# Kernel tuning notes

Measured on AMD Instinct MI355X. Metric: run time of the kernel, lower is better.

The kernel has to match this reference:

```python
import jax, jax.numpy as jnp
import numpy as np

# Static config (matches init_kwargs)
B, S = 4, 1024            # prefill: 4 sequences of 1024 tokens (num_tokens = 4096)
H = 16                    # num_heads
NOPE, ROPE, VD = 128, 64, 128
RANK = 512                # kv_lora_rank
SCALE = 0.07216878364870323  # 1/sqrt(head_dim=192)


def setup_inputs() -> dict:
    key = jax.random.key(0)
    k1, k2, k3, k4 = jax.random.split(key, 4)
    T = B * S
    return {
        "q": jax.random.normal(k1, (T, H, NOPE + ROPE), dtype=jnp.float32),
        "compressed_kv": jax.random.normal(k2, (T, RANK), dtype=jnp.float32),
        "rope_k": jax.random.normal(k3, (T, ROPE), dtype=jnp.float32),
        "w_up": jax.random.normal(k4, (H * (NOPE + VD), RANK), dtype=jnp.float32) * 0.02,
    }


def reference(q, compressed_kv, rope_k, w_up):
    T = q.shape[0]
    # Up-project latent -> per-head (k_nope, v): [T, H, NOPE+VD]
    kv = (compressed_kv @ w_up.T).reshape(B, S, H, NOPE + VD)
    k_nope = kv[..., :NOPE]          # [B,S,H,NOPE]
    v = kv[..., NOPE:]               # [B,S,H,VD]

    qb = q.reshape(B, S, H, NOPE + ROPE)
    q_nope = qb[..., :NOPE]          # [B,S,H,NOPE]
    q_rope = qb[..., NOPE:]          # [B,S,H,ROPE]
    rk = rope_k.reshape(B, S, ROPE)  # head-shared RoPE K component

    # Attention logits: nope part (per-head K) + rope part (shared K)
    scores = jnp.einsum('bqhd,bkhd->bhqk', q_nope, k_nope)
    scores = scores + jnp.einsum('bqhd,bkd->bhqk', q_rope, rk)
    scores = scores * SCALE

    # Causal mask within each sequence
    causal = jnp.tril(jnp.ones((S, S), dtype=bool))
    scores = jnp.where(causal[None, None], scores, jnp.finfo(scores.dtype).min)

    p = jax.nn.softmax(scores, axis=-1)                 # [B,H,S,S]
    out = jnp.einsum('bhqk,bkhd->bqhd', p, v)           # [B,S,H,VD]
    return out.reshape(T, H, VD)
```

## Files before the change

kernel.cpp:

```cpp
#include <hip/hip_runtime.h>
#include <stdint.h>


#define Hz 16
#define Sz 1024
#define RANKz 512
#define SCALEf 0.07216878364870323f

typedef unsigned short u16;
typedef __attribute__((ext_vector_type(8))) short bf16x8;
typedef __attribute__((ext_vector_type(4))) float f32x4;
typedef __attribute__((ext_vector_type(16))) float f32x16;

__device__ __forceinline__ u16 f2b(float f) {
  union { float f; uint32_t u; } x; x.f = f;
  return (u16)((x.u + 0x7fffu + ((x.u >> 16) & 1u)) >> 16);
}
__device__ __forceinline__ uint32_t cvtpk(float lo, float hi_) {
  uint32_t r;
  asm("v_cvt_pk_bf16_f32 %0, %1, %2" : "=v"(r) : "v"(lo), "v"(hi_));
  return r;
}

__global__ void cvt_bf16_kernel(const float* __restrict__ a, u16* __restrict__ ao,
                                const float* __restrict__ b, u16* __restrict__ bo,
                                const float* __restrict__ c, u16* __restrict__ co,
                                int na, int nb) {
  int idx = blockIdx.x * blockDim.x + threadIdx.x;
  const float* s; u16* d; int i;
  if (idx < na)            { s = a; d = ao; i = idx; }
  else if (idx < na + nb)  { s = b; d = bo; i = idx - na; }
  else                     { s = c; d = co; i = idx - na - nb; }
  float4 v = ((const float4*)s)[i];
  ushort4 o = make_ushort4(f2b(v.x), f2b(v.y), f2b(v.z), f2b(v.w));
  ((ushort4*)d)[i] = o;
}

__global__ __launch_bounds__(256)
void gemm_kv_bf16(const u16* __restrict__ A,
                  const u16* __restrict__ Bm,
                  u16* __restrict__ C) {
  __shared__ u16 As[128 * 32];
  __shared__ u16 Bs[128 * 32];
  const int tid = threadIdx.x;
  const int w = tid >> 6, lane = tid & 63;
  const int wr = w >> 1, wc = w & 1;
  const int row0 = blockIdx.x * 128, col0 = blockIdx.y * 128;
  f32x4 acc[4][4];
#pragma unroll
  for (int m = 0; m < 4; ++m)
#pragma unroll
    for (int n = 0; n < 4; ++n) acc[m][n] = (f32x4){0.f, 0.f, 0.f, 0.f};

  const int rstage = (lane >> 2);
  const int cstage = (lane & 3) * 8;

  for (int kt = 0; kt < RANKz / 32; ++kt) {
    const int k0 = kt * 32;
#pragma unroll
    for (int i = 0; i < 2; ++i) {
      const int chunk = i * 4 + w;
      const int r = chunk * 16 + rstage;
      const u16* ga = A  + (size_t)(row0 + r) * RANKz + k0 + cstage;
      const u16* gb = Bm + (size_t)(col0 + r) * RANKz + k0 + cstage;
      __builtin_amdgcn_global_load_lds((const __attribute__((address_space(1))) void*)ga,
                                       (__attribute__((address_space(3))) void*)&As[chunk * 512], 16, 0, 0);
      __builtin_amdgcn_global_load_lds((const __attribute__((address_space(1))) void*)gb,
                                       (__attribute__((address_space(3))) void*)&Bs[chunk * 512], 16, 0, 0);
    }
    __syncthreads();
    const int klo = (lane >> 4) * 8;
    bf16x8 af[4], bfr[4];
#pragma unroll
    for (int m = 0; m < 4; ++m)
      af[m] = *(const bf16x8*)&As[(wr * 64 + m * 16 + (lane & 15)) * 32 + klo];
#pragma unroll
    for (int n = 0; n < 4; ++n)
      bfr[n] = *(const bf16x8*)&Bs[(wc * 64 + n * 16 + (lane & 15)) * 32 + klo];
#pragma unroll
    for (int m = 0; m < 4; ++m)
#pragma unroll
      for (int n = 0; n < 4; ++n)
        acc[m][n] = __builtin_amdgcn_mfma_f32_16x16x32_bf16(af[m], bfr[n], acc[m][n], 0, 0, 0);
    __syncthreads();
  }
  const int cb = col0 + wc * 64 + (lane & 15);
  const int rb = row0 + wr * 64 + (lane >> 4) * 4;
#pragma unroll
  for (int m = 0; m < 4; ++m)
#pragma unroll
    for (int n = 0; n < 4; ++n)
#pragma unroll
      for (int j = 0; j < 4; ++j)
        C[(size_t)(rb + m * 16 + j) * 4096 + (cb + n * 16)] = f2b(acc[m][n][j]);
}

__global__ __launch_bounds__(512, 2)
void mla_attn_mfma(const float* __restrict__ q,
                   const u16* __restrict__ kvb,
                   const u16* __restrict__ ropeb,
                   float* __restrict__ out) {
  __shared__ __align__(16) unsigned char LB[131072];

  const int tid = threadIdx.x;
  const int w = tid >> 6, lane = tid & 63;
  const int l31 = lane & 31, hi = lane >> 5;
  const int half = w >> 2, strip = w & 3;

  const int bid = blockIdx.x;
  const int job = (bid & 7) * 32 + (bid >> 3);
  const int bh = job >> 2, pr = job & 3;
  const int bat = bh >> 4, h = bh & 15;
  const int tok0 = bat * Sz;

  const int vkp = tid & 63, vdc = (tid >> 6) & 7;

#pragma unroll 1
  for (int pass = 0; pass < 2; ++pass) {
    const int qt = pass ? pr : (7 - pr);
    const int ntiles = qt + 1;
    const int q0 = qt * 128 + strip * 32;

    bf16x8 qf[12];
    {
      const float* qp = q + ((size_t)(tok0 + q0 + l31) * Hz + h) * 192 + hi * 8;
#pragma unroll
      for (int ds = 0; ds < 12; ++ds) {
        float4 a = *(const float4*)(qp + ds * 16);
        float4 b = *(const float4*)(qp + ds * 16 + 4);
        union { bf16x8 v; u16 u[8]; } t;
        t.u[0] = f2b(a.x * SCALEf); t.u[1] = f2b(a.y * SCALEf);
        t.u[2] = f2b(a.z * SCALEf); t.u[3] = f2b(a.w * SCALEf);
        t.u[4] = f2b(b.x * SCALEf); t.u[5] = f2b(b.y * SCALEf);
        t.u[6] = f2b(b.z * SCALEf); t.u[7] = f2b(b.w * SCALEf);
        qf[ds] = t.v;
      }
    }

    f32x16 acc[4];
#pragma unroll
    for (int db = 0; db < 4; ++db)
#pragma unroll
      for (int r = 0; r < 16; ++r) acc[db][r] = 0.f;
    float m_run = -1e30f, l_run = 0.f;

    uint4 va0, va1, vb0, vb1;

    {
      const int tokt = tok0;
#pragma unroll
      for (int i = 0; i < 4; ++i) {
        const int c = w * 4 + i;
        const int row = c * 4 + (lane >> 4);
        const int sc = (lane & 15) ^ (row & 7);
        const u16* src = kvb + ((size_t)(tokt + row) * Hz + h) * 256 + sc * 8;
        __builtin_amdgcn_global_load_lds((const __attribute__((address_space(1))) void*)src,
                                         (__attribute__((address_space(3))) void*)(LB + c * 1024), 16, 0, 0);
      }
#pragma unroll
      for (int i = 0; i < 2; ++i) {
        const int c = w * 2 + i;
        const int row = c * 8 + (lane >> 3);
        const int sc = (lane & 7) ^ (row & 7);
        const u16* src = ropeb + (size_t)(tokt + row) * 64 + sc * 8;
        __builtin_amdgcn_global_load_lds((const __attribute__((address_space(1))) void*)src,
                                         (__attribute__((address_space(3))) void*)(LB + 65536 + c * 1024), 16, 0, 0);
      }
      const u16* vp = kvb + ((size_t)(tokt + vkp * 2) * Hz + h) * 256 + 128 + vdc * 16;
      va0 = *(const uint4*)(vp);
      va1 = *(const uint4*)(vp + 8);
      vb0 = *(const uint4*)(vp + Hz * 256);
      vb1 = *(const uint4*)(vp + Hz * 256 + 8);
    }
    __syncthreads();
    {
      union { uint4 v; u16 u[8]; } A0, A1, B0, B1;
      A0.v = va0; A1.v = va1; B0.v = vb0; B1.v = vb1;
      char* vt = (char*)(LB + 98304);
      const int inb = (4 * vkp) & 15, cc = vkp >> 2;
#pragma unroll
      for (int i = 0; i < 8; ++i) {
        { const int d = vdc * 16 + i;
          uint32_t wv = (uint32_t)A0.u[i] | ((uint32_t)B0.u[i] << 16);
          *(uint32_t*)(vt + d * 256 + 16 * (cc ^ (d & 7)) + inb) = wv; }
        { const int d = vdc * 16 + 8 + i;
          uint32_t wv = (uint32_t)A1.u[i] | ((uint32_t)B1.u[i] << 16);
          *(uint32_t*)(vt + d * 256 + 16 * (cc ^ (d & 7)) + inb) = wv; }
      }
    }
    __syncthreads();

#pragma unroll 1
    for (int t = 0; t < ntiles; ++t) {
      const int cur = t & 1;
      const bool havenext = (t + 1 < ntiles);
      if (havenext) {
        const int tokt = tok0 + (t + 1) * 128;
#pragma unroll
        for (int i = 0; i < 4; ++i) {
          const int c = w * 4 + i;
          const int row = c * 4 + (lane >> 4);
          const int sc = (lane & 15) ^ (row & 7);
          const u16* src = kvb + ((size_t)(tokt + row) * Hz + h) * 256 + sc * 8;
          __builtin_amdgcn_global_load_lds((const __attribute__((address_space(1))) void*)src,
                                           (__attribute__((address_space(3))) void*)(LB + (cur ^ 1) * 32768 + c * 1024), 16, 0, 0);
        }
#pragma unroll
        for (int i = 0; i < 2; ++i) {
          const int c = w * 2 + i;
          const int row = c * 8 + (lane >> 3);
          const int sc = (lane & 7) ^ (row & 7);
          const u16* src = ropeb + (size_t)(tokt + row) * 64 + sc * 8;
          __builtin_amdgcn_global_load_lds((const __attribute__((address_space(1))) void*)src,
                                           (__attribute__((address_space(3))) void*)(LB + 65536 + (cur ^ 1) * 16384 + c * 1024), 16, 0, 0);
        }
        const u16* vp = kvb + ((size_t)(tokt + vkp * 2) * Hz + h) * 256 + 128 + vdc * 16;
        va0 = *(const uint4*)(vp);
        va1 = *(const uint4*)(vp + 8);
        vb0 = *(const uint4*)(vp + Hz * 256);
        vb1 = *(const uint4*)(vp + Hz * 256 + 8);
      }

      const bool active = (t * 128 + half * 64) <= (q0 + 31);
      if (active) {
        const u16* KnC = (const u16*)(LB + cur * 32768);
        const u16* KrC = (const u16*)(LB + 65536 + cur * 16384);
        f32x16 s0, s1;
#pragma unroll
        for (int r = 0; r < 16; ++r) { s0[r] = 0.f; s1[r] = 0.f; }
        const int row_a = half * 64 + l31;
        const int row_b = row_a + 32;
#pragma unroll
        for (int ds = 0; ds < 8; ++ds) {
          bf16x8 k0v = *(const bf16x8*)&KnC[row_a * 128 + 8 * ((2 * ds + hi) ^ (row_a & 7))];
          bf16x8 k1v = *(const bf16x8*)&KnC[row_b * 128 + 8 * ((2 * ds + hi) ^ (row_b & 7))];
          s0 = __builtin_amdgcn_mfma_f32_32x32x16_bf16(k0v, qf[ds], s0, 0, 0, 0);
          s1 = __builtin_amdgcn_mfma_f32_32x32x16_bf16(k1v, qf[ds], s1, 0, 0, 0);
        }
#pragma unroll
        for (int ds = 8; ds < 12; ++ds) {
          bf16x8 k0v = *(const bf16x8*)&KrC[row_a * 64 + 8 * ((2 * (ds - 8) + hi) ^ (row_a & 7))];
          bf16x8 k1v = *(const bf16x8*)&KrC[row_b * 64 + 8 * ((2 * (ds - 8) + hi) ^ (row_b & 7))];
          s0 = __builtin_amdgcn_mfma_f32_32x32x16_bf16(k0v, qf[ds], s0, 0, 0, 0);
          s1 = __builtin_amdgcn_mfma_f32_32x32x16_bf16(k1v, qf[ds], s1, 0, 0, 0);
        }

        if (t == qt) {
          const int qg = q0 + l31;
          const int kb0 = t * 128 + half * 64;
#pragma unroll
          for (int r = 0; r < 16; ++r) {
            const int cr_ = (r & 3) + 8 * (r >> 2) + 4 * hi;
            if (kb0 + cr_ > qg)      s0[r] = -1e30f;
            if (kb0 + 32 + cr_ > qg) s1[r] = -1e30f;
          }
        }

        float mx = -1e30f;
#pragma unroll
        for (int r = 0; r < 16; ++r) { mx = fmaxf(mx, s0[r]); mx = fmaxf(mx, s1[r]); }
        mx = fmaxf(mx, __shfl_xor(mx, 32));
        const bool need = __any(mx > m_run + 8.f);
        if (need) {
          const float nm = fmaxf(m_run, mx);
          const float cr = __expf(m_run - nm);
          m_run = nm; l_run *= cr;
#pragma unroll
          for (int r = 0; r < 16; ++r) {
            const float crg = __shfl(cr, (r & 3) + 8 * (r >> 2) + 4 * hi);
#pragma unroll
            for (int db = 0; db < 4; ++db) acc[db][r] *= crg;
          }
        }
        float ts = 0.f;
#pragma unroll
        for (int r = 0; r < 16; ++r) {
          s0[r] = __expf(s0[r] - m_run); ts += s0[r];
          s1[r] = __expf(s1[r] - m_run); ts += s1[r];
        }
        ts += __shfl_xor(ts, 32);
        l_run += ts;

        bf16x8 pf[4];
#pragma unroll
        for (int ks = 0; ks < 4; ++ks) {
          const int o = (ks & 1) * 8;
          uint32_t w0, w1, w2, w3;
          if (ks < 2) {
            w0 = cvtpk(s0[o + 0], s0[o + 1]); w1 = cvtpk(s0[o + 4], s0[o + 5]);
            w2 = cvtpk(s0[o + 2], s0[o + 3]); w3 = cvtpk(s0[o + 6], s0[o + 7]);
          } else {
            w0 = cvtpk(s1[o + 0], s1[o + 1]); w1 = cvtpk(s1[o + 4], s1[o + 5]);
            w2 = cvtpk(s1[o + 2], s1[o + 3]); w3 = cvtpk(s1[o + 6], s1[o + 7]);
          }
          const uint32_t t0 = __shfl_xor(w0, 32), t1 = __shfl_xor(w1, 32);
          const uint32_t t2 = __shfl_xor(w2, 32), t3 = __shfl_xor(w3, 32);
          union { bf16x8 v; uint32_t u[4]; } P;
          P.u[0] = hi ? t1 : w0;
          P.u[1] = hi ? t3 : w2;
          P.u[2] = hi ? w1 : t0;
          P.u[3] = hi ? w3 : t2;
          pf[ks] = P.v;
        }

        const u16* VtC = (const u16*)(LB + 98304);
#pragma unroll
        for (int ks = 0; ks < 4; ++ks)
#pragma unroll
          for (int db = 0; db < 4; ++db) {
            const int row = db * 32 + l31;
            bf16x8 vf = *(const bf16x8*)&VtC[row * 128 + 8 * ((half * 8 + 2 * ks + hi) ^ (row & 7))];
            acc[db] = __builtin_amdgcn_mfma_f32_32x32x16_bf16(pf[ks], vf, acc[db], 0, 0, 0);
          }
      }

      __syncthreads();
      if (havenext) {
        union { uint4 v; u16 u[8]; } A0, A1, B0, B1;
        A0.v = va0; A1.v = va1; B0.v = vb0; B1.v = vb1;
        char* vt = (char*)(LB + 98304);
        const int inb = (4 * vkp) & 15, cc = vkp >> 2;
#pragma unroll
        for (int i = 0; i < 8; ++i) {
          { const int d = vdc * 16 + i;
            uint32_t wv = (uint32_t)A0.u[i] | ((uint32_t)B0.u[i] << 16);
            *(uint32_t*)(vt + d * 256 + 16 * (cc ^ (d & 7)) + inb) = wv; }
          { const int d = vdc * 16 + 8 + i;
            uint32_t wv = (uint32_t)A1.u[i] | ((uint32_t)B1.u[i] << 16);
            *(uint32_t*)(vt + d * 256 + 16 * (cc ^ (d & 7)) + inb) = wv; }
        }
        __syncthreads();
      }
    }

    float* mb = (float*)LB;
    float* ml = (float*)(LB + 65536);
    if (half == 1) {
#pragma unroll
      for (int db = 0; db < 4; ++db)
#pragma unroll
        for (int q4 = 0; q4 < 4; ++q4) {
          float4 v = make_float4(acc[db][q4 * 4 + 0], acc[db][q4 * 4 + 1],
                                 acc[db][q4 * 4 + 2], acc[db][q4 * 4 + 3]);
          *(float4*)&mb[strip * 4096 + db * 1024 + q4 * 256 + lane * 4] = v;
        }
      if (lane < 32) { ml[strip * 64 + lane] = m_run; ml[strip * 64 + 32 + lane] = l_run; }
    }
    __syncthreads();
    if (half == 0) {
      const float mp = ml[strip * 64 + l31];
      const float lp = ml[strip * 64 + 32 + l31];
      const float M  = fmaxf(m_run, mp);
      const float sA = __expf(m_run - M);
      const float sB = __expf(mp - M);
      const float inv = 1.0f / (l_run * sA + lp * sB);
      const float fAl = sA * inv, fBl = sB * inv;
      float fA[16], fB[16];
#pragma unroll
      for (int r = 0; r < 16; ++r) {
        const int cr_ = (r & 3) + 8 * (r >> 2) + 4 * hi;
        fA[r] = __shfl(fAl, cr_);
        fB[r] = __shfl(fBl, cr_);
      }
#pragma unroll
      for (int db = 0; db < 4; ++db)
#pragma unroll
        for (int q4 = 0; q4 < 4; ++q4) {
          float4 pv = *(const float4*)&mb[strip * 4096 + db * 1024 + q4 * 256 + lane * 4];
#pragma unroll
          for (int jj = 0; jj < 4; ++jj) {
            const int r = q4 * 4 + jj;
            const int cr_ = (r & 3) + 8 * (r >> 2) + 4 * hi;
            const float pvj = (jj == 0) ? pv.x : (jj == 1) ? pv.y : (jj == 2) ? pv.z : pv.w;
            out[((size_t)(tok0 + q0 + cr_) * Hz + h) * 128 + db * 32 + l31] =
                acc[db][r] * fA[r] + pvj * fB[r];
          }
        }
    }
    __syncthreads();
  }
}

extern "C" void kernel_launch(void* const* d_in, const int* in_sizes, int n_in,
                              void* d_out, int out_size, void* d_ws, size_t ws_size,
                              hipStream_t stream) {
  const float* q    = (const float*)d_in[0];
  const float* ckv  = (const float*)d_in[1];
  const float* rope = (const float*)d_in[2];
  const float* wup  = (const float*)d_in[3];
  float* out = (float*)d_out;

  u16* ckvb  = (u16*)d_ws;
  u16* wupb  = ckvb + (size_t)4096 * RANKz;
  u16* kvb   = wupb + (size_t)4096 * RANKz;
  u16* ropeb = kvb + (size_t)4096 * 4096;

  const int nvec = 4096 * RANKz / 4;
  const int nrope = 4096 * 64 / 4;
  cvt_bf16_kernel<<<(2 * nvec + nrope) / 256, 256, 0, stream>>>(ckv, ckvb, wup, wupb, rope, ropeb, nvec, nvec);

  dim3 gg(32, 32);
  gemm_kv_bf16<<<gg, 256, 0, stream>>>(ckvb, wupb, kvb);

  mla_attn_mfma<<<256, 512, 0, stream>>>(q, kvb, ropeb, out);
}
```

Before: 90.00 us.

## Split attention key tile across four wave quarters with 1024-thread blocks

Doubles the attention block to 16 waves so each wave handles 32 keys of a 128-key tile instead of 64. The four partial softmax/PV results per query strip are then merged through LDS in a two-step tree, with partials stored as bf16. Wave priority is raised around the MFMA sections. The aim is more waves in flight to hide latency, at the cost of extra merge work, lower-precision partials, and tighter register limits that could cause spills.

```diff
diff --git a/kernel.cpp b/kernel.cpp
--- a/kernel.cpp
+++ b/kernel.cpp
@@ -6,6 +6,7 @@
 #define Sz 1024
 #define RANKz 512
 #define SCALEf 0.07216878364870323f
+#define CRr(r) ((((r) & 3)) + 8 * ((r) >> 2) + 4 * hi)
 
 typedef unsigned short u16;
 typedef __attribute__((ext_vector_type(8))) short bf16x8;
@@ -15,6 +16,10 @@
 __device__ __forceinline__ u16 f2b(float f) {
   union { float f; uint32_t u; } x; x.f = f;
   return (u16)((x.u + 0x7fffu + ((x.u >> 16) & 1u)) >> 16);
+}
+__device__ __forceinline__ float b2f(u16 s) {
+  union { uint32_t u; float f; } x; x.u = ((uint32_t)s) << 16;
+  return x.f;
 }
 __device__ __forceinline__ uint32_t cvtpk(float lo, float hi_) {
   uint32_t r;
@@ -95,7 +100,7 @@
         C[(size_t)(rb + m * 16 + j) * 4096 + (cb + n * 16)] = f2b(acc[m][n][j]);
 }
 
-__global__ __launch_bounds__(512, 2)
+__global__ __launch_bounds__(1024, 4)
 void mla_attn_mfma(const float* __restrict__ q,
                    const u16* __restrict__ kvb,
                    const u16* __restrict__ ropeb,
@@ -105,7 +110,7 @@
   const int tid = threadIdx.x;
   const int w = tid >> 6, lane = tid & 63;
   const int l31 = lane & 31, hi = lane >> 5;
-  const int half = w >> 2, strip = w & 3;
+  const int quarter = w >> 2, strip = w & 3;
 
   const int bid = blockIdx.x;
   const int job = (bid & 7) * 32 + (bid >> 3);
@@ -113,7 +118,92 @@
   const int bat = bh >> 4, h = bh & 15;
   const int tok0 = bat * Sz;
 
-  const int vkp = tid & 63, vdc = (tid >> 6) & 7;
+  const int vkp = tid & 63, vdc = tid >> 6;
+  uint4 va, vb;
+
+  float m_run, l_run;
+  f32x16 acc[4];
+
+  auto stageK = [&](int tokt, int buf) {
+#pragma unroll
+    for (int i = 0; i < 2; ++i) {
+      const int c = w * 2 + i;
+      const int row = c * 4 + (lane >> 4);
+      const int sc = (lane & 15) ^ (row & 7);
+      const u16* src = kvb + ((size_t)(tokt + row) * Hz + h) * 256 + sc * 8;
+      __builtin_amdgcn_global_load_lds((const __attribute__((address_space(1))) void*)src,
+                                       (__attribute__((address_space(3))) void*)(LB + buf * 32768 + c * 1024), 16, 0, 0);
+    }
+    {
+      const int c = w;
+      const int row = c * 8 + (lane >> 3);
+      const int sc = (lane & 7) ^ (row & 7);
+      const u16* src = ropeb + (size_t)(tokt + row) * 64 + sc * 8;
+      __builtin_amdgcn_global_load_lds((const __attribute__((address_space(1))) void*)src,
+                                       (__attribute__((address_space(3))) void*)(LB + 65536 + buf * 16384 + c * 1024), 16, 0, 0);
+    }
+  };
+  auto loadV = [&](int tokt) {
+    const u16* vp = kvb + ((size_t)(tokt + vkp * 2) * Hz + h) * 256 + 128 + vdc * 8;
+    va = *(const uint4*)vp;
+    vb = *(const uint4*)(vp + 4096);
+  };
+  auto writeVt = [&]() {
+    union { uint4 v; u16 u[8]; } A_, B_;
+    A_.v = va; B_.v = vb;
+    uint32_t* vt = (uint32_t*)(LB + 98304);
+#pragma unroll
+    for (int i = 0; i < 8; ++i) {
+      const int d = vdc * 8 + i;
+      vt[d * 64 + 4 * ((vkp >> 2) ^ (d & 7)) + (vkp & 3)] =
+          (uint32_t)A_.u[i] | ((uint32_t)B_.u[i] << 16);
+    }
+  };
+  auto writePartial = [&](uint32_t* bp, float* mlp) {
+    if (hi == 0) {
+      mlp[strip * 64 + l31 * 2]     = m_run;
+      mlp[strip * 64 + l31 * 2 + 1] = l_run;
+    }
+#pragma unroll
+    for (int db = 0; db < 4; ++db) {
+      const int d = db * 32 + l31;
+#pragma unroll
+      for (int g = 0; g < 4; ++g) {
+        uint2 pk;
+        pk.x = cvtpk(acc[db][g * 4 + 0], acc[db][g * 4 + 1]);
+        pk.y = cvtpk(acc[db][g * 4 + 2], acc[db][g * 4 + 3]);
+        *(uint2*)&bp[strip * 2048 + d * 16 + ((g * 4 + 2 * hi) ^ ((d & 7) << 1))] = pk;
+      }
+    }
+  };
+  auto mergeIn = [&](const uint32_t* bp, const float* mlp) {
+    const float m_p = mlp[strip * 64 + l31 * 2];
+    const float l_p = mlp[strip * 64 + l31 * 2 + 1];
+    const float M = fmaxf(m_run, m_p);
+    const float sA = __expf(m_run - M), sB = __expf(m_p - M);
+    l_run = l_run * sA + l_p * sB;
+    m_run = M;
+    float fa[16], fb[16];
+#pragma unroll
+    for (int r = 0; r < 16; ++r) { fa[r] = __shfl(sA, CRr(r)); fb[r] = __shfl(sB, CRr(r)); }
+#pragma unroll
+    for (int db = 0; db < 4; ++db) {
+      const int d = db * 32 + l31;
+#pragma unroll
+      for (int g = 0; g < 4; ++g) {
+        uint2 pk = *(const uint2*)&bp[strip * 2048 + d * 16 + ((g * 4 + 2 * hi) ^ ((d & 7) << 1))];
+        acc[db][g * 4 + 0] = acc[db][g * 4 + 0] * fa[g * 4 + 0] + b2f((u16)(pk.x & 0xffffu)) * fb[g * 4 + 0];
+        acc[db][g * 4 + 1] = acc[db][g * 4 + 1] * fa[g * 4 + 1] + b2f((u16)(pk.x >> 16))     * fb[g * 4 + 1];
+        acc[db][g * 4 + 2] = acc[db][g * 4 + 2] * fa[g * 4 + 2] + b2f((u16)(pk.y & 0xffffu)) * fb[g * 4 + 2];
+        acc[db][g * 4 + 3] = acc[db][g * 4 + 3] * fa[g * 4 + 3] + b2f((u16)(pk.y >> 16))     * fb[g * 4 + 3];
+      }
+    }
+  };
+
+  uint32_t* buf0 = (uint32_t*)LB;
+  uint32_t* buf1 = (uint32_t*)(LB + 32768);
+  float* mlA = (float*)(LB + 98304);
+  float* mlB = (float*)(LB + 98304 + 1024);
 
 #pragma unroll 1
   for (int pass = 0; pass < 2; ++pass) {
@@ -137,57 +227,16 @@
       }
     }
 
-    f32x16 acc[4];
 #pragma unroll
     for (int db = 0; db < 4; ++db)
 #pragma unroll
       for (int r = 0; r < 16; ++r) acc[db][r] = 0.f;
-    float m_run = -1e30f, l_run = 0.f;
-
-    uint4 va0, va1, vb0, vb1;
-
-    {
-      const int tokt = tok0;
-#pragma unroll
-      for (int i = 0; i < 4; ++i) {
-        const int c = w * 4 + i;
-        const int row = c * 4 + (lane >> 4);
-        const int sc = (lane & 15) ^ (row & 7);
-        const u16* src = kvb + ((size_t)(tokt + row) * Hz + h) * 256 + sc * 8;
-        __builtin_amdgcn_global_load_lds((const __attribute__((address_space(1))) void*)src,
-                                         (__attribute__((address_space(3))) void*)(LB + c * 1024), 16, 0, 0);
-      }
-#pragma unroll
-      for (int i = 0; i < 2; ++i) {
-        const int c = w * 2 + i;
-        const int row = c * 8 + (lane >> 3);
-        const int sc = (lane & 7) ^ (row & 7);
-        const u16* src = ropeb + (size_t)(tokt + row) * 64 + sc * 8;
-        __builtin_amdgcn_global_load_lds((const __attribute__((address_space(1))) void*)src,
-                                         (__attribute__((address_space(3))) void*)(LB + 65536 + c * 1024), 16, 0, 0);
-      }
-      const u16* vp = kvb + ((size_t)(tokt + vkp * 2) * Hz + h) * 256 + 128 + vdc * 16;
-      va0 = *(const uint4*)(vp);
-      va1 = *(const uint4*)(vp + 8);
-      vb0 = *(const uint4*)(vp + Hz * 256);
-      vb1 = *(const uint4*)(vp + Hz * 256 + 8);
-    }
-    __syncthreads();
-    {
-      union { uint4 v; u16 u[8]; } A0, A1, B0, B1;
-      A0.v = va0; A1.v = va1; B0.v = vb0; B1.v = vb1;
-      char* vt = (char*)(LB + 98304);
-      const int inb = (4 * vkp) & 15, cc = vkp >> 2;
-#pragma unroll
-      for (int i = 0; i < 8; ++i) {
-        { const int d = vdc * 16 + i;
-          uint32_t wv = (uint32_t)A0.u[i] | ((uint32_t)B0.u[i] << 16);
-          *(uint32_t*)(vt + d * 256 + 16 * (cc ^ (d & 7)) + inb) = wv; }
-        { const int d = vdc * 16 + 8 + i;
-          uint32_t wv = (uint32_t)A1.u[i] | ((uint32_t)B1.u[i] << 16);
-          *(uint32_t*)(vt + d * 256 + 16 * (cc ^ (d & 7)) + inb) = wv; }
-      }
-    }
+    m_run = -1e30f; l_run = 0.f;
+
+    stageK(tok0, 0);
+    loadV(tok0);
+    __syncthreads();
+    writeVt();
     __syncthreads();
 
 #pragma unroll 1
@@ -195,104 +244,68 @@
       const int cur = t & 1;
       const bool havenext = (t + 1 < ntiles);
       if (havenext) {
-        const int tokt = tok0 + (t + 1) * 128;
-#pragma unroll
-        for (int i = 0; i < 4; ++i) {
-          const int c = w * 4 + i;
-          const int row = c * 4 + (lane >> 4);
-          const int sc = (lane & 15) ^ (row & 7);
-          const u16* src = kvb + ((size_t)(tokt + row) * Hz + h) * 256 + sc * 8;
-          __builtin_amdgcn_global_load_lds((const __attribute__((address_space(1))) void*)src,
-                                           (__attribute__((address_space(3))) void*)(LB + (cur ^ 1) * 32768 + c * 1024), 16, 0, 0);
-        }
-#pragma unroll
-        for (int i = 0; i < 2; ++i) {
-          const int c = w * 2 + i;
-          const int row = c * 8 + (lane >> 3);
-          const int sc = (lane & 7) ^ (row & 7);
-          const u16* src = ropeb + (size_t)(tokt + row) * 64 + sc * 8;
-          __builtin_amdgcn_global_load_lds((const __attribute__((address_space(1))) void*)src,
-                                           (__attribute__((address_space(3))) void*)(LB + 65536 + (cur ^ 1) * 16384 + c * 1024), 16, 0, 0);
-        }
-        const u16* vp = kvb + ((size_t)(tokt + vkp * 2) * Hz + h) * 256 + 128 + vdc * 16;
-        va0 = *(const uint4*)(vp);
-        va1 = *(const uint4*)(vp + 8);
-        vb0 = *(const uint4*)(vp + Hz * 256);
-        vb1 = *(const uint4*)(vp + Hz * 256 + 8);
-      }
-
-      const bool active = (t * 128 + half * 64) <= (q0 + 31);
+        stageK(tok0 + (t + 1) * 128, cur ^ 1);
+        loadV(tok0 + (t + 1) * 128);
+      }
+
+      const bool active = (t * 128 + quarter * 32) <= (q0 + 31);
       if (active) {
         const u16* KnC = (const u16*)(LB + cur * 32768);
         const u16* KrC = (const u16*)(LB + 65536 + cur * 16384);
-        f32x16 s0, s1;
-#pragma unroll
-        for (int r = 0; r < 16; ++r) { s0[r] = 0.f; s1[r] = 0.f; }
-        const int row_a = half * 64 + l31;
-        const int row_b = row_a + 32;
+        const int row_a = quarter * 32 + l31;
+        const int swz = row_a & 7;
+
+        f32x16 s0;
+#pragma unroll
+        for (int r = 0; r < 16; ++r) s0[r] = 0.f;
+        __builtin_amdgcn_s_setprio(1);
 #pragma unroll
         for (int ds = 0; ds < 8; ++ds) {
-          bf16x8 k0v = *(const bf16x8*)&KnC[row_a * 128 + 8 * ((2 * ds + hi) ^ (row_a & 7))];
-          bf16x8 k1v = *(const bf16x8*)&KnC[row_b * 128 + 8 * ((2 * ds + hi) ^ (row_b & 7))];
-          s0 = __builtin_amdgcn_mfma_f32_32x32x16_bf16(k0v, qf[ds], s0, 0, 0, 0);
-          s1 = __builtin_amdgcn_mfma_f32_32x32x16_bf16(k1v, qf[ds], s1, 0, 0, 0);
+          bf16x8 kf = *(const bf16x8*)&KnC[row_a * 128 + 8 * ((2 * ds + hi) ^ swz)];
+          s0 = __builtin_amdgcn_mfma_f32_32x32x16_bf16(kf, qf[ds], s0, 0, 0, 0);
         }
 #pragma unroll
         for (int ds = 8; ds < 12; ++ds) {
-          bf16x8 k0v = *(const bf16x8*)&KrC[row_a * 64 + 8 * ((2 * (ds - 8) + hi) ^ (row_a & 7))];
-          bf16x8 k1v = *(const bf16x8*)&KrC[row_b * 64 + 8 * ((2 * (ds - 8) + hi) ^ (row_b & 7))];
-          s0 = __builtin_amdgcn_mfma_f32_32x32x16_bf16(k0v, qf[ds], s0, 0, 0, 0);
-          s1 = __builtin_amdgcn_mfma_f32_32x32x16_bf16(k1v, qf[ds], s1, 0, 0, 0);
-        }
-
-        if (t == qt) {
-          const int qg = q0 + l31;
-          const int kb0 = t * 128 + half * 64;
-#pragma unroll
-          for (int r = 0; r < 16; ++r) {
-            const int cr_ = (r & 3) + 8 * (r >> 2) + 4 * hi;
-            if (kb0 + cr_ > qg)      s0[r] = -1e30f;
-            if (kb0 + 32 + cr_ > qg) s1[r] = -1e30f;
-          }
-        }
-
-        float mx = -1e30f;
-#pragma unroll
-        for (int r = 0; r < 16; ++r) { mx = fmaxf(mx, s0[r]); mx = fmaxf(mx, s1[r]); }
+          bf16x8 kf = *(const bf16x8*)&KrC[row_a * 64 + 8 * ((2 * (ds - 8) + hi) ^ swz)];
+          s0 = __builtin_amdgcn_mfma_f32_32x32x16_bf16(kf, qf[ds], s0, 0, 0, 0);
+        }
+        __builtin_amdgcn_s_setprio(0);
+
+        if (t == qt && quarter == strip) {
+#pragma unroll
+          for (int r = 0; r < 16; ++r)
+            if (CRr(r) > l31) s0[r] = -1e30f;
+        }
+
+        float mx = s0[0];
+#pragma unroll
+        for (int r = 1; r < 16; ++r) mx = fmaxf(mx, s0[r]);
         mx = fmaxf(mx, __shfl_xor(mx, 32));
-        const bool need = __any(mx > m_run + 8.f);
-        if (need) {
+        if (__any(mx > m_run + 8.f)) {
           const float nm = fmaxf(m_run, mx);
           const float cr = __expf(m_run - nm);
           m_run = nm; l_run *= cr;
 #pragma unroll
           for (int r = 0; r < 16; ++r) {
-            const float crg = __shfl(cr, (r & 3) + 8 * (r >> 2) + 4 * hi);
+            const float crg = __shfl(cr, CRr(r));
 #pragma unroll
             for (int db = 0; db < 4; ++db) acc[db][r] *= crg;
           }
         }
         float ts = 0.f;
 #pragma unroll
-        for (int r = 0; r < 16; ++r) {
-          s0[r] = __expf(s0[r] - m_run); ts += s0[r];
-          s1[r] = __expf(s1[r] - m_run); ts += s1[r];
-        }
+        for (int r = 0; r < 16; ++r) { s0[r] = __expf(s0[r] - m_run); ts += s0[r]; }
         ts += __shfl_xor(ts, 32);
         l_run += ts;
 
-        bf16x8 pf[4];
-#pragma unroll
-        for (int ks = 0; ks < 4; ++ks) {
-          const int o = (ks & 1) * 8;
-          uint32_t w0, w1, w2, w3;
-          if (ks < 2) {
-            w0 = cvtpk(s0[o + 0], s0[o + 1]); w1 = cvtpk(s0[o + 4], s0[o + 5]);
-            w2 = cvtpk(s0[o + 2], s0[o + 3]); w3 = cvtpk(s0[o + 6], s0[o + 7]);
-          } else {
-            w0 = cvtpk(s1[o + 0], s1[o + 1]); w1 = cvtpk(s1[o + 4], s1[o + 5]);
-            w2 = cvtpk(s1[o + 2], s1[o + 3]); w3 = cvtpk(s1[o + 6], s1[o + 7]);
-          }
+        bf16x8 pf[2];
+#pragma unroll
+        for (int ks = 0; ks < 2; ++ks) {
+          const int o = ks * 8;
+          const uint32_t w0 = cvtpk(s0[o + 0], s0[o + 1]);
+          const uint32_t w1 = cvtpk(s0[o + 4], s0[o + 5]);
+          const uint32_t w2 = cvtpk(s0[o + 2], s0[o + 3]);
+          const uint32_t w3 = cvtpk(s0[o + 6], s0[o + 7]);
           const uint32_t t0 = __shfl_xor(w0, 32), t1 = __shfl_xor(w1, 32);
           const uint32_t t2 = __shfl_xor(w2, 32), t3 = __shfl_xor(w3, 32);
           union { bf16x8 v; uint32_t u[4]; } P;
@@ -304,78 +317,44 @@
         }
 
         const u16* VtC = (const u16*)(LB + 98304);
-#pragma unroll
-        for (int ks = 0; ks < 4; ++ks)
+        __builtin_amdgcn_s_setprio(1);
+#pragma unroll
+        for (int ks = 0; ks < 2; ++ks)
 #pragma unroll
           for (int db = 0; db < 4; ++db) {
-            const int row = db * 32 + l31;
-            bf16x8 vf = *(const bf16x8*)&VtC[row * 128 + 8 * ((half * 8 + 2 * ks + hi) ^ (row & 7))];
+            const int d = db * 32 + l31;
+            bf16x8 vf = *(const bf16x8*)&VtC[d * 128 + 8 * ((quarter * 4 + 2 * ks + hi) ^ (d & 7))];
             acc[db] = __builtin_amdgcn_mfma_f32_32x32x16_bf16(pf[ks], vf, acc[db], 0, 0, 0);
           }
+        __builtin_amdgcn_s_setprio(0);
       }
 
       __syncthreads();
       if (havenext) {
-        union { uint4 v; u16 u[8]; } A0, A1, B0, B1;
-        A0.v = va0; A1.v = va1; B0.v = vb0; B1.v = vb1;
-        char* vt = (char*)(LB + 98304);
-        const int inb = (4 * vkp) & 15, cc = vkp >> 2;
-#pragma unroll
-        for (int i = 0; i < 8; ++i) {
-          { const int d = vdc * 16 + i;
-            uint32_t wv = (uint32_t)A0.u[i] | ((uint32_t)B0.u[i] << 16);
-            *(uint32_t*)(vt + d * 256 + 16 * (cc ^ (d & 7)) + inb) = wv; }
-          { const int d = vdc * 16 + 8 + i;
-            uint32_t wv = (uint32_t)A1.u[i] | ((uint32_t)B1.u[i] << 16);
-            *(uint32_t*)(vt + d * 256 + 16 * (cc ^ (d & 7)) + inb) = wv; }
-        }
+        writeVt();
         __syncthreads();
       }
     }
 
-    float* mb = (float*)LB;
-    float* ml = (float*)(LB + 65536);
-    if (half == 1) {
+    if (quarter == 1) writePartial(buf0, mlA);
+    if (quarter == 3) writePartial(buf1, mlB);
+    __syncthreads();
+    if (quarter == 0) mergeIn(buf0, mlA);
+    if (quarter == 2) mergeIn(buf1, mlB);
+    __syncthreads();
+    if (quarter == 2) writePartial(buf0, mlA);
+    __syncthreads();
+    if (quarter == 0) {
+      mergeIn(buf0, mlA);
+      const float inv = 1.0f / l_run;
+      float fi[16];
+#pragma unroll
+      for (int r = 0; r < 16; ++r) fi[r] = __shfl(inv, CRr(r));
 #pragma unroll
       for (int db = 0; db < 4; ++db)
 #pragma unroll
-        for (int q4 = 0; q4 < 4; ++q4) {
-          float4 v = make_float4(acc[db][q4 * 4 + 0], acc[db][q4 * 4 + 1],
-                                 acc[db][q4 * 4 + 2], acc[db][q4 * 4 + 3]);
-          *(float4*)&mb[strip * 4096 + db * 1024 + q4 * 256 + lane * 4] = v;
-        }
-      if (lane < 32) { ml[strip * 64 + lane] = m_run; ml[strip * 64 + 32 + lane] = l_run; }
-    }
-    __syncthreads();
-    if (half == 0) {
-      const float mp = ml[strip * 64 + l31];
-      const float lp = ml[strip * 64 + 32 + l31];
-      const float M  = fmaxf(m_run, mp);
-      const float sA = __expf(m_run - M);
-      const float sB = __expf(mp - M);
-      const float inv = 1.0f / (l_run * sA + lp * sB);
-      const float fAl = sA * inv, fBl = sB * inv;
-      float fA[16], fB[16];
-#pragma unroll
-      for (int r = 0; r < 16; ++r) {
-        const int cr_ = (r & 3) + 8 * (r >> 2) + 4 * hi;
-        fA[r] = __shfl(fAl, cr_);
-        fB[r] = __shfl(fBl, cr_);
-      }
-#pragma unroll
-      for (int db = 0; db < 4; ++db)
-#pragma unroll
-        for (int q4 = 0; q4 < 4; ++q4) {
-          float4 pv = *(const float4*)&mb[strip * 4096 + db * 1024 + q4 * 256 + lane * 4];
-#pragma unroll
-          for (int jj = 0; jj < 4; ++jj) {
-            const int r = q4 * 4 + jj;
-            const int cr_ = (r & 3) + 8 * (r >> 2) + 4 * hi;
-            const float pvj = (jj == 0) ? pv.x : (jj == 1) ? pv.y : (jj == 2) ? pv.z : pv.w;
-            out[((size_t)(tok0 + q0 + cr_) * Hz + h) * 128 + db * 32 + l31] =
-                acc[db][r] * fA[r] + pvj * fB[r];
-          }
-        }
+        for (int r = 0; r < 16; ++r)
+          out[((size_t)(tok0 + q0 + CRr(r)) * Hz + h) * 128 + db * 32 + l31] = acc[db][r] * fi[r];
     }
     __syncthreads();
   }
@@ -402,5 +381,5 @@
   dim3 gg(32, 32);
   gemm_kv_bf16<<<gg, 256, 0, stream>>>(ckvb, wupb, kvb);
 
-  mla_attn_mfma<<<256, 512, 0, stream>>>(q, kvb, ropeb, out);
-}
+  mla_attn_mfma<<<256, 1024, 0, stream>>>(q, kvb, ropeb, out);
+}
```

New measurement: 257.7 us. +186.3%, slower.

## Batch LDS fragment loads before MFMA runs with setprio and relax launch bounds

Applied to the files above, without the earlier changes.

Restructures the attention inner loop so K and V fragments are loaded from LDS into register arrays in batches, followed by bursts of MFMAs wrapped in s_setprio to raise wave priority during matrix work. The V global loads are issued before the LDS-direct loads, the row max uses a tree reduction, and launch bounds drop from 2 to 1 waves-per-EU minimum. The aim is to hide LDS latency and interleave waves better. The cost is higher register pressure, which the relaxed launch bounds allow, possibly at the expense of occupancy.

```diff
diff --git a/kernel.cpp b/kernel.cpp
--- a/kernel.cpp
+++ b/kernel.cpp
@@ -95,7 +95,7 @@
         C[(size_t)(rb + m * 16 + j) * 4096 + (cb + n * 16)] = f2b(acc[m][n][j]);
 }
 
-__global__ __launch_bounds__(512, 2)
+__global__ __launch_bounds__(512, 1)
 void mla_attn_mfma(const float* __restrict__ q,
                    const u16* __restrict__ kvb,
                    const u16* __restrict__ ropeb,
@@ -148,6 +148,11 @@
 
     {
       const int tokt = tok0;
+      const u16* vp = kvb + ((size_t)(tokt + vkp * 2) * Hz + h) * 256 + 128 + vdc * 16;
+      va0 = *(const uint4*)(vp);
+      va1 = *(const uint4*)(vp + 8);
+      vb0 = *(const uint4*)(vp + Hz * 256);
+      vb1 = *(const uint4*)(vp + Hz * 256 + 8);
 #pragma unroll
       for (int i = 0; i < 4; ++i) {
         const int c = w * 4 + i;
@@ -166,11 +171,6 @@
         __builtin_amdgcn_global_load_lds((const __attribute__((address_space(1))) void*)src,
                                          (__attribute__((address_space(3))) void*)(LB + 65536 + c * 1024), 16, 0, 0);
       }
-      const u16* vp = kvb + ((size_t)(tokt + vkp * 2) * Hz + h) * 256 + 128 + vdc * 16;
-      va0 = *(const uint4*)(vp);
-      va1 = *(const uint4*)(vp + 8);
-      vb0 = *(const uint4*)(vp + Hz * 256);
-      vb1 = *(const uint4*)(vp + Hz * 256 + 8);
     }
     __syncthreads();
     {
@@ -196,6 +196,11 @@
       const bool havenext = (t + 1 < ntiles);
       if (havenext) {
         const int tokt = tok0 + (t + 1) * 128;
+        const u16* vp = kvb + ((size_t)(tokt + vkp * 2) * Hz + h) * 256 + 128 + vdc * 16;
+        va0 = *(const uint4*)(vp);
+        va1 = *(const uint4*)(vp + 8);
+        vb0 = *(const uint4*)(vp + Hz * 256);
+        vb1 = *(const uint4*)(vp + Hz * 256 + 8);
 #pragma unroll
         for (int i = 0; i < 4; ++i) {
           const int c = w * 4 + i;
@@ -214,36 +219,49 @@
           __builtin_amdgcn_global_load_lds((const __attribute__((address_space(1))) void*)src,
                                            (__attribute__((address_space(3))) void*)(LB + 65536 + (cur ^ 1) * 16384 + c * 1024), 16, 0, 0);
         }
-        const u16* vp = kvb + ((size_t)(tokt + vkp * 2) * Hz + h) * 256 + 128 + vdc * 16;
-        va0 = *(const uint4*)(vp);
-        va1 = *(const uint4*)(vp + 8);
-        vb0 = *(const uint4*)(vp + Hz * 256);
-        vb1 = *(const uint4*)(vp + Hz * 256 + 8);
       }
 
       const bool active = (t * 128 + half * 64) <= (q0 + 31);
       if (active) {
         const u16* KnC = (const u16*)(LB + cur * 32768);
         const u16* KrC = (const u16*)(LB + 65536 + cur * 16384);
-        f32x16 s0, s1;
-#pragma unroll
-        for (int r = 0; r < 16; ++r) { s0[r] = 0.f; s1[r] = 0.f; }
         const int row_a = half * 64 + l31;
         const int row_b = row_a + 32;
-#pragma unroll
-        for (int ds = 0; ds < 8; ++ds) {
-          bf16x8 k0v = *(const bf16x8*)&KnC[row_a * 128 + 8 * ((2 * ds + hi) ^ (row_a & 7))];
-          bf16x8 k1v = *(const bf16x8*)&KnC[row_b * 128 + 8 * ((2 * ds + hi) ^ (row_b & 7))];
-          s0 = __builtin_amdgcn_mfma_f32_32x32x16_bf16(k0v, qf[ds], s0, 0, 0, 0);
-          s1 = __builtin_amdgcn_mfma_f32_32x32x16_bf16(k1v, qf[ds], s1, 0, 0, 0);
-        }
-#pragma unroll
-        for (int ds = 8; ds < 12; ++ds) {
-          bf16x8 k0v = *(const bf16x8*)&KrC[row_a * 64 + 8 * ((2 * (ds - 8) + hi) ^ (row_a & 7))];
-          bf16x8 k1v = *(const bf16x8*)&KrC[row_b * 64 + 8 * ((2 * (ds - 8) + hi) ^ (row_b & 7))];
-          s0 = __builtin_amdgcn_mfma_f32_32x32x16_bf16(k0v, qf[ds], s0, 0, 0, 0);
-          s1 = __builtin_amdgcn_mfma_f32_32x32x16_bf16(k1v, qf[ds], s1, 0, 0, 0);
-        }
+        const int swz = row_a & 7;
+
+        f32x16 s0, s1;
+#pragma unroll
+        for (int r = 0; r < 16; ++r) { s0[r] = 0.f; s1[r] = 0.f; }
+        bf16x8 ka[6], kb[6];
+#pragma unroll
+        for (int ds = 0; ds < 6; ++ds) {
+          ka[ds] = *(const bf16x8*)&KnC[row_a * 128 + 8 * ((2 * ds + hi) ^ swz)];
+          kb[ds] = *(const bf16x8*)&KnC[row_b * 128 + 8 * ((2 * ds + hi) ^ swz)];
+        }
+        __builtin_amdgcn_s_setprio(1);
+#pragma unroll
+        for (int ds = 0; ds < 6; ++ds) {
+          s0 = __builtin_amdgcn_mfma_f32_32x32x16_bf16(ka[ds], qf[ds], s0, 0, 0, 0);
+          s1 = __builtin_amdgcn_mfma_f32_32x32x16_bf16(kb[ds], qf[ds], s1, 0, 0, 0);
+        }
+        __builtin_amdgcn_s_setprio(0);
+#pragma unroll
+        for (int ds = 0; ds < 2; ++ds) {
+          ka[ds] = *(const bf16x8*)&KnC[row_a * 128 + 8 * ((2 * (ds + 6) + hi) ^ swz)];
+          kb[ds] = *(const bf16x8*)&KnC[row_b * 128 + 8 * ((2 * (ds + 6) + hi) ^ swz)];
+        }
+#pragma unroll
+        for (int ds = 0; ds < 4; ++ds) {
+          ka[2 + ds] = *(const bf16x8*)&KrC[row_a * 64 + 8 * ((2 * ds + hi) ^ swz)];
+          kb[2 + ds] = *(const bf16x8*)&KrC[row_b * 64 + 8 * ((2 * ds + hi) ^ swz)];
+        }
+        __builtin_amdgcn_s_setprio(1);
+#pragma unroll
+        for (int ds = 0; ds < 6; ++ds) {
+          s0 = __builtin_amdgcn_mfma_f32_32x32x16_bf16(ka[ds], qf[6 + ds], s0, 0, 0, 0);
+          s1 = __builtin_amdgcn_mfma_f32_32x32x16_bf16(kb[ds], qf[6 + ds], s1, 0, 0, 0);
+        }
+        __builtin_amdgcn_s_setprio(0);
 
         if (t == qt) {
           const int qg = q0 + l31;
@@ -256,9 +274,16 @@
           }
         }
 
-        float mx = -1e30f;
-#pragma unroll
-        for (int r = 0; r < 16; ++r) { mx = fmaxf(mx, s0[r]); mx = fmaxf(mx, s1[r]); }
+        float mp0 = fmaxf(s0[0], s0[1]),  mp1 = fmaxf(s0[2], s0[3]);
+        float mp2 = fmaxf(s0[4], s0[5]),  mp3 = fmaxf(s0[6], s0[7]);
+        float mp4 = fmaxf(s0[8], s0[9]),  mp5 = fmaxf(s0[10], s0[11]);
+        float mp6 = fmaxf(s0[12], s0[13]), mp7 = fmaxf(s0[14], s0[15]);
+        mp0 = fmaxf(mp0, fmaxf(s1[0], s1[1]));   mp1 = fmaxf(mp1, fmaxf(s1[2], s1[3]));
+        mp2 = fmaxf(mp2, fmaxf(s1[4], s1[5]));   mp3 = fmaxf(mp3, fmaxf(s1[6], s1[7]));
+        mp4 = fmaxf(mp4, fmaxf(s1[8], s1[9]));   mp5 = fmaxf(mp5, fmaxf(s1[10], s1[11]));
+        mp6 = fmaxf(mp6, fmaxf(s1[12], s1[13])); mp7 = fmaxf(mp7, fmaxf(s1[14], s1[15]));
+        float mx = fmaxf(fmaxf(fmaxf(mp0, mp1), fmaxf(mp2, mp3)),
+                         fmaxf(fmaxf(mp4, mp5), fmaxf(mp6, mp7)));
         mx = fmaxf(mx, __shfl_xor(mx, 32));
         const bool need = __any(mx > m_run + 8.f);
         if (need) {
@@ -304,14 +329,35 @@
         }
 
         const u16* VtC = (const u16*)(LB + 98304);
-#pragma unroll
-        for (int ks = 0; ks < 4; ++ks)
+        bf16x8 vfr[8];
+#pragma unroll
+        for (int ks = 0; ks < 2; ++ks)
 #pragma unroll
           for (int db = 0; db < 4; ++db) {
             const int row = db * 32 + l31;
-            bf16x8 vf = *(const bf16x8*)&VtC[row * 128 + 8 * ((half * 8 + 2 * ks + hi) ^ (row & 7))];
-            acc[db] = __builtin_amdgcn_mfma_f32_32x32x16_bf16(pf[ks], vf, acc[db], 0, 0, 0);
-          }
+            vfr[ks * 4 + db] = *(const bf16x8*)&VtC[row * 128 + 8 * ((half * 8 + 2 * ks + hi) ^ (row & 7))];
+          }
+        __builtin_amdgcn_s_setprio(1);
+#pragma unroll
+        for (int ks = 0; ks < 2; ++ks)
+#pragma unroll
+          for (int db = 0; db < 4; ++db)
+            acc[db] = __builtin_amdgcn_mfma_f32_32x32x16_bf16(pf[ks], vfr[ks * 4 + db], acc[db], 0, 0, 0);
+        __builtin_amdgcn_s_setprio(0);
+#pragma unroll
+        for (int ks = 0; ks < 2; ++ks)
+#pragma unroll
+          for (int db = 0; db < 4; ++db) {
+            const int row = db * 32 + l31;
+            vfr[ks * 4 + db] = *(const bf16x8*)&VtC[row * 128 + 8 * ((half * 8 + 2 * (ks + 2) + hi) ^ (row & 7))];
+          }
+        __builtin_amdgcn_s_setprio(1);
+#pragma unroll
+        for (int ks = 0; ks < 2; ++ks)
+#pragma unroll
+          for (int db = 0; db < 4; ++db)
+            acc[db] = __builtin_amdgcn_mfma_f32_32x32x16_bf16(pf[ks + 2], vfr[ks * 4 + db], acc[db], 0, 0, 0);
+        __builtin_amdgcn_s_setprio(0);
       }
 
       __syncthreads();
```

Measured after the change: 110.1 us. 22.3% more time.
